# Optimization experiments

Hardware: AMD Instinct MI355X
Metric: run time of the kernel (lower is better)

## Reference

```python
import math
import jax
import jax.numpy as jnp
import numpy as np
from jax import lax

Q = 64          # num_quantiles (init default)
EPS = 1e-8      # eps (init default)


def setup_inputs() -> dict:
    key = jax.random.key(0)
    B, T, C = 64, 4096, 128
    x = jax.random.normal(key, (B, T, C), dtype=jnp.float32)
    return {"x": x}


def _build_quantile_table(x):
    """x: (B,T,C) -> quantiles (B,C,Q), levels (Q,). Unmasked branch."""
    B, T, C = x.shape
    levels = jnp.linspace(0.5 / Q, 1.0 - 0.5 / Q, Q, dtype=x.dtype)
    x_sorted = jnp.sort(x, axis=1)                      # (B,T,C) sorted over time
    positions = jnp.clip(levels * T - 0.5, 0.0, float(T - 1))   # (Q,)
    pos_int = jnp.clip(positions.astype(jnp.int32), 0, T - 2)   # (Q,)
    pos_frac = jnp.clip(positions - pos_int.astype(x.dtype), 0.0, 1.0)
    x_bct = jnp.transpose(x_sorted, (0, 2, 1))          # (B,C,T)
    q0 = x_bct[..., pos_int]                            # (B,C,Q)
    q1 = x_bct[..., jnp.minimum(pos_int + 1, T - 1)]    # (B,C,Q)
    quantiles = q0 * (1.0 - pos_frac) + q1 * pos_frac
    return quantiles, levels


def _interp_cdf(x_bc, q_bc, levels):
    """Piecewise-linear F_X(x): x_bc (N,T), q_bc (N,Q) monotone, levels (Q,)."""
    # batched searchsorted (right) per row
    idx = jax.vmap(lambda a, v: jnp.searchsorted(a, v, side="right"))(q_bc, x_bc)
    idx = jnp.clip(idx, 1, Q - 1)                       # (N,T)
    x0 = jnp.take_along_axis(q_bc, idx - 1, axis=-1)
    x1 = jnp.take_along_axis(q_bc, idx, axis=-1)
    y0 = levels[idx - 1]
    y1 = levels[idx]
    slope = (y1 - y0) / jnp.maximum(x1 - x0, 1e-12)
    return y0 + slope * (x_bc - x0)


def _probit(p):
    p_safe = jnp.clip(p, 1e-6, 1.0 - 1e-6)
    return jax.scipy.special.erfinv(2.0 * p_safe - 1.0) * math.sqrt(2.0)


def reference(x):
    B, T, C = x.shape
    quantiles, levels = _build_quantile_table(x)
    # torch detaches the quantile table: gradients flow through x only
    quantiles = lax.stop_gradient(quantiles)
    x_bc = jnp.transpose(x, (0, 2, 1)).reshape(B * C, T)
    q_bc = quantiles.reshape(B * C, Q)
    p_bc = jnp.clip(_interp_cdf(x_bc, q_bc, levels), EPS, 1.0 - EPS)
    z_bc = _probit(p_bc)
    return jnp.transpose(z_bc.reshape(B, C, T), (0, 2, 1))
```

## Files before the change

### kernel.cpp

```cpp
#include <hip/hip_runtime.h>
#include <math.h>

#define BB 64
#define TT 4096
#define CC 128
#define NQ 64
#define TCH2 128
#define NBKT 2048
#define NBKT_G 1024

__global__ __launch_bounds__(256) void transpose_kernel(const float* __restrict__ x,
                                                        float* __restrict__ xT) {
    __shared__ float tile[64][65];
    const int cb = blockIdx.x;
    const int tb = blockIdx.y;
    const int b  = blockIdx.z;
    const int tid = threadIdx.x;
    const int q = tid >> 6;
    const int l = tid & 63;

    const float* xs = x + ((size_t)b * TT + (size_t)tb * 64) * CC + (size_t)cb * 64;
    #pragma unroll
    for (int j = 0; j < 16; ++j) {
        int tl = q * 16 + j;
        tile[tl][l] = xs[(size_t)tl * CC + l];
    }
    __syncthreads();
    float* xd = xT + ((size_t)b * CC + (size_t)cb * 64) * TT + (size_t)tb * 64;
    #pragma unroll
    for (int j = 0; j < 16; ++j) {
        int cl = q * 16 + j;
        xd[(size_t)cl * TT + l] = tile[l][cl];
    }
}

__global__ __launch_bounds__(256) void bucket_quantile_T(const float* __restrict__ xT,
                                                         float* __restrict__ qtab) {
    __shared__ unsigned       A[NBKT];
    __shared__ unsigned short cum16[NBKT + 2];
    __shared__ unsigned char  flag8[NBKT];
    __shared__ unsigned short rankinfo[128];
    __shared__ unsigned short pb16[132];
    __shared__ unsigned       cur2[132];
    __shared__ unsigned       wsum[4], wsum2[4];

    const int row = blockIdx.x;
    const float* xrow = xT + (size_t)row * TT;
    const int tid = threadIdx.x, lane = tid & 63, wid = tid >> 6;

    float vv[16];
    #pragma unroll
    for (int j = 0; j < 4; ++j) {
        float4 v4 = ((const float4*)xrow)[j * 256 + tid];
        vv[j * 4 + 0] = v4.x; vv[j * 4 + 1] = v4.y;
        vv[j * 4 + 2] = v4.z; vv[j * 4 + 3] = v4.w;
    }

    *(uint4*)&A[tid * 8]      = make_uint4(0u, 0u, 0u, 0u);
    *(uint4*)&A[tid * 8 + 4]  = make_uint4(0u, 0u, 0u, 0u);
    *(uint2*)&flag8[tid * 8]  = make_uint2(~0u, ~0u);
    __syncthreads();

    #pragma unroll
    for (int j = 0; j < 16; ++j) {
        int bk = (int)((vv[j] + 5.0f) * 204.8f);
        bk = bk < 0 ? 0 : (bk > NBKT - 1 ? NBKT - 1 : bk);
        atomicAdd(&A[bk], 1u);
    }
    __syncthreads();

    uint4 h0 = *(uint4*)&A[tid * 8];
    uint4 h1 = *(uint4*)&A[tid * 8 + 4];
    unsigned S = h0.x + h0.y + h0.z + h0.w + h1.x + h1.y + h1.z + h1.w;
    unsigned incl = S;
    #pragma unroll
    for (int off = 1; off < 64; off <<= 1) {
        unsigned n = __shfl_up(incl, off, 64);
        if (lane >= off) incl += n;
    }
    if (lane == 63) wsum[wid] = incl;
    __syncthreads();
    unsigned base = incl - S;
    for (int w = 0; w < wid; ++w) base += wsum[w];

    unsigned carr[9];
    carr[0] = base;
    carr[1] = carr[0] + h0.x; carr[2] = carr[1] + h0.y;
    carr[3] = carr[2] + h0.z; carr[4] = carr[3] + h0.w;
    carr[5] = carr[4] + h1.x; carr[6] = carr[5] + h1.y;
    carr[7] = carr[6] + h1.z; carr[8] = carr[7] + h1.w;
    #pragma unroll
    for (int bi = 0; bi < 8; ++bi)
        cum16[tid * 8 + bi] = (unsigned short)carr[bi];
    if (tid == 255) cum16[NBKT] = (unsigned short)TT;

    unsigned flg = 0, myLen = 0, myCnt = 0;
    #pragma unroll
    for (int bi = 0; bi < 8; ++bi) {
        const int cs = (int)carr[bi], ce = (int)carr[bi + 1];
        if (ce > cs) {
            int t0 = cs - 32;
            int q0 = t0 < 0 ? 0 : (t0 >> 6);
            int q1 = (ce >> 6); if (q1 > 63) q1 = 63;
            bool any = false;
            for (int q = q0; q <= q1; ++q) {
                int r1 = (q << 6) + 31, r2 = r1 + 1;
                bool i1 = (r1 >= cs) && (r1 < ce);
                bool i2 = (r2 >= cs) && (r2 < ce);
                if (i1) rankinfo[2 * q]     = (unsigned short)(tid * 8 + bi);
                if (i2) rankinfo[2 * q + 1] = (unsigned short)(tid * 8 + bi);
                any |= (i1 || i2);
            }
            if (any) { flg |= (1u << bi); myLen += (unsigned)(ce - cs); myCnt++; }
        }
    }

    unsigned pk = (myLen << 16) | myCnt;
    unsigned incl2 = pk;
    #pragma unroll
    for (int off = 1; off < 64; off <<= 1) {
        unsigned n = __shfl_up(incl2, off, 64);
        if (lane >= off) incl2 += n;
    }
    if (lane == 63) wsum2[wid] = incl2;
    __syncthreads();
    unsigned b2 = incl2 - pk;
    for (int w = 0; w < wid; ++w) b2 += wsum2[w];
    unsigned lenB = b2 >> 16, cntB = b2 & 0xFFFFu;
    #pragma unroll
    for (int bi = 0; bi < 8; ++bi) {
        if (flg & (1u << bi)) {
            int s = tid * 8 + bi;
            flag8[s] = (unsigned char)cntB;
            pb16[cntB] = (unsigned short)lenB;
            cur2[cntB] = lenB;
            cntB++;
            lenB += carr[bi + 1] - carr[bi];
        }
    }
    __syncthreads();

    #pragma unroll
    for (int j = 0; j < 16; ++j) {
        int bk = (int)((vv[j] + 5.0f) * 204.8f);
        bk = bk < 0 ? 0 : (bk > NBKT - 1 ? NBKT - 1 : bk);
        unsigned char fl = flag8[bk];
        if (fl != 0xFFu) {
            unsigned p = atomicAdd(&cur2[fl], 1u);
            if (p < (unsigned)NBKT) ((float*)A)[p] = vv[j];
        }
    }
    __syncthreads();

    if (tid < 128) {
        const int j = tid;
        const int r = ((j >> 1) << 6) + 31 + (j & 1);
        const int s = rankinfo[j];
        const int cs = (int)cum16[s];
        const int L = (int)cum16[s + 1] - cs;
        const int k = r - cs;
        const unsigned char fid = flag8[s];
        const float* seg = (const float*)A + pb16[fid];

        float ans = 0.0f;
        for (int i = 0; i < L; ++i) {
            float vi = seg[i];
            int rk = 0;
            for (int jj = 0; jj < L; ++jj) {
                float vj = seg[jj];
                rk += (vj < vi) || (vj == vi && jj < i);
            }
            if (rk == k) { ans = vi; break; }
        }
        float vo = __shfl_xor(ans, 1, 64);
        if ((tid & 1) == 0)
            qtab[(size_t)row * NQ + (j >> 1)] = (ans + vo) * 0.5f;
    }
}

__global__ __launch_bounds__(256) void bucket_quantile_G(const float* __restrict__ x,
                                                         float* __restrict__ qtab) {
    __shared__ unsigned hist[NBKT_G];
    __shared__ unsigned cum[NBKT_G];
    __shared__ unsigned cur[NBKT_G];
    __shared__ float    pool[TT];
    __shared__ unsigned wsum[4];

    const int bid = blockIdx.x;
    const int row = ((bid & 7) << 10) | (bid >> 3);
    const int b = row >> 7, c = row & (CC - 1);
    const float* xrow = x + (size_t)b * TT * CC + c;
    const int tid = threadIdx.x;
    const int lane = tid & 63, wid = tid >> 6;

    float vv[16];
    #pragma unroll
    for (int j = 0; j < 16; ++j)
        vv[j] = xrow[(size_t)((j << 8) + tid) * CC];

    *(uint4*)&hist[tid << 2] = make_uint4(0u, 0u, 0u, 0u);
    __syncthreads();

    #pragma unroll
    for (int j = 0; j < 16; ++j) {
        int bk = (int)((vv[j] + 5.0f) * 102.4f);
        bk = bk < 0 ? 0 : (bk > NBKT_G - 1 ? NBKT_G - 1 : bk);
        atomicAdd(&hist[bk], 1u);
    }
    __syncthreads();

    uint4 h = *(uint4*)&hist[tid << 2];
    unsigned S = h.x + h.y + h.z + h.w;
    unsigned incl = S;
    #pragma unroll
    for (int off = 1; off < 64; off <<= 1) {
        unsigned n = __shfl_up(incl, off, 64);
        if (lane >= off) incl += n;
    }
    if (lane == 63) wsum[wid] = incl;
    __syncthreads();
    unsigned base = incl - S;
    for (int w = 0; w < wid; ++w) base += wsum[w];
    {
        unsigned c0 = base, c1 = c0 + h.x, c2 = c1 + h.y, c3 = c2 + h.z;
        *(uint4*)&cum[tid << 2] = make_uint4(c0, c1, c2, c3);
        *(uint4*)&cur[tid << 2] = make_uint4(c0, c1, c2, c3);
    }
    __syncthreads();

    #pragma unroll
    for (int j = 0; j < 16; ++j) {
        int bk = (int)((vv[j] + 5.0f) * 102.4f);
        bk = bk < 0 ? 0 : (bk > NBKT_G - 1 ? NBKT_G - 1 : bk);
        unsigned p = atomicAdd(&cur[bk], 1u);
        pool[p] = vv[j];
    }
    __syncthreads();

    if (tid < 128) {
        const int q = tid >> 1;
        const int r = (q << 6) + 31 + (tid & 1);
        int pos = 0;
        #pragma unroll
        for (int step = 512; step >= 1; step >>= 1) {
            int np = pos + step;
            if (np <= NBKT_G - 1 && (int)cum[np] <= r) pos = np;
        }
        const int segbase = (int)cum[pos];
        const int L = (int)hist[pos];
        const int k = r - segbase;
        const float* seg = &pool[segbase];

        float ans = 0.0f;
        for (int i = 0; i < L; ++i) {
            float vi = seg[i];
            int rk = 0;
            for (int jj = 0; jj < L; ++jj) {
                float vj = seg[jj];
                rk += (vj < vi) || (vj == vi && jj < i);
            }
            if (rk == k) { ans = vi; break; }
        }
        float vo = __shfl_xor(ans, 1, 64);
        if ((tid & 1) == 0)
            qtab[(size_t)row * NQ + q] = (ans + vo) * 0.5f;
    }
}

__global__ __launch_bounds__(256) void apply_kernel(const float* __restrict__ x,
                                                    const float* __restrict__ qtab,
                                                    float* __restrict__ out) {
    __shared__ float qtT[NQ][64];
    const int b   = blockIdx.x;
    const int tch = blockIdx.y;
    const int ch  = blockIdx.z;
    const int tid = threadIdx.x;

    const float* qsrc = qtab + ((size_t)b * CC + (size_t)ch * 64) * NQ;
    for (int i = tid; i < 64 * NQ; i += 256) {
        int cl = i >> 6, k = i & 63;
        qtT[k][cl ^ k] = qsrc[i];
    }
    __syncthreads();

    const int c0   = (tid & 15) * 4;
    const int trow = tid >> 4;
    const size_t base = (size_t)b * TT * CC + (size_t)tch * TCH2 * CC
                      + (size_t)ch * 64;
    const float* xp = x + base;
    float* op = out + base;
    const float invq = 1.0f / (float)NQ;

    #pragma unroll
    for (int g = 0; g < 4; ++g) {
        const int ta = trow + 16 * (2 * g);
        const int tb = trow + 16 * (2 * g + 1);
        const int offa = ta * CC + c0;
        const int offb = tb * CC + c0;
        float4 va = *(const float4*)(xp + offa);
        float4 vb = *(const float4*)(xp + offb);

        float v[8] = { va.x, va.y, va.z, va.w, vb.x, vb.y, vb.z, vb.w };
        int   cc[8];
        int   pos[8];
        #pragma unroll
        for (int e = 0; e < 8; ++e) { cc[e] = c0 + (e & 3); pos[e] = 0; }

        #pragma unroll
        for (int step = 32; step >= 1; step >>= 1) {
            float pr[8];
            #pragma unroll
            for (int e = 0; e < 8; ++e) {
                int np = pos[e] + step - 1;
                pr[e] = qtT[np][cc[e] ^ np];
            }
            #pragma unroll
            for (int e = 0; e < 8; ++e)
                if (pr[e] <= v[e]) pos[e] += step;
        }

        float x0[8], x1[8];
        #pragma unroll
        for (int e = 0; e < 8; ++e) {
            int idx = pos[e];
            idx = idx < 1 ? 1 : (idx > NQ - 1 ? NQ - 1 : idx);
            pos[e] = idx;
            x0[e] = qtT[idx - 1][cc[e] ^ (idx - 1)];
            x1[e] = qtT[idx][cc[e] ^ idx];
        }

        float r[8];
        #pragma unroll
        for (int e = 0; e < 8; ++e) {
            const float y0 = ((float)pos[e] - 0.5f) * invq;
            const float rcp = __builtin_amdgcn_rcpf(fmaxf(x1[e] - x0[e], 1e-12f));
            float p = fmaf(invq * rcp, v[e] - x0[e], y0);
            p = fminf(fmaxf(p, 1e-6f), 1.0f - 1e-6f);

            const float xx = 2.0f * p - 1.0f;
            float w = -__logf((1.0f - xx) * (1.0f + xx));
            float z;
            if (w < 5.0f) {
                float ww = w - 2.5f;
                z = 2.81022636e-08f;
                z = fmaf(z, ww, 3.43273939e-07f);
                z = fmaf(z, ww, -3.5233877e-06f);
                z = fmaf(z, ww, -4.39150654e-06f);
                z = fmaf(z, ww, 0.00021858087f);
                z = fmaf(z, ww, -0.00125372503f);
                z = fmaf(z, ww, -0.00417768164f);
                z = fmaf(z, ww, 0.246640727f);
                z = fmaf(z, ww, 1.50140941f);
            } else {
                float ww = sqrtf(w) - 3.0f;
                z = -0.000200214257f;
                z = fmaf(z, ww, 0.000100950558f);
                z = fmaf(z, ww, 0.00134934322f);
                z = fmaf(z, ww, -0.00367342844f);
                z = fmaf(z, ww, 0.00573950773f);
                z = fmaf(z, ww, -0.0076224613f);
                z = fmaf(z, ww, 0.00943887047f);
                z = fmaf(z, ww, 1.00167406f);
                z = fmaf(z, ww, 2.83297682f);
            }
            r[e] = z * xx * 1.4142135623730951f;
        }

        *(float4*)(op + offa) = make_float4(r[0], r[1], r[2], r[3]);
        *(float4*)(op + offb) = make_float4(r[4], r[5], r[6], r[7]);
    }
}

extern "C" void kernel_launch(void* const* d_in, const int* in_sizes, int n_in,
                              void* d_out, int out_size, void* d_ws, size_t ws_size,
                              hipStream_t stream) {
    const float* x = (const float*)d_in[0];
    float* out = (float*)d_out;
    float* qtab = (float*)d_ws;
    const size_t qtab_bytes = (size_t)BB * CC * NQ * 4;
    const size_t xT_bytes   = (size_t)BB * CC * TT * 4;

    if (ws_size >= qtab_bytes + xT_bytes) {
        float* xT = (float*)((char*)d_ws + qtab_bytes);
        dim3 tgrid(2, 64, BB);
        transpose_kernel<<<tgrid, 256, 0, stream>>>(x, xT);
        bucket_quantile_T<<<BB * CC, 256, 0, stream>>>(xT, qtab);
    } else {
        bucket_quantile_G<<<BB * CC, 256, 0, stream>>>(x, qtab);
    }
    dim3 grid(BB, TT / TCH2, 2);
    apply_kernel<<<grid, 256, 0, stream>>>(x, qtab, out);
}
```

Baseline: 216.7 us.

## Shrink quantile blocks to 128 threads, reload row instead of holding registers

The bucket-quantile kernel now runs with 128 threads per row, each handling 16 histogram bins and 32 values. The values are read from global memory a second time in the scatter pass instead of being kept in registers. The cumulative-count table is removed by packing each bin's index and in-bin rank into rankinfo, with bin lengths stored in a new len8 array. The aim is lower shared memory and register use per block for better occupancy and fewer barriers, at the cost of a second global read of each row and less parallelism within a block.

```diff
diff --git a/kernel.cpp b/kernel.cpp
--- a/kernel.cpp
+++ b/kernel.cpp
@@ -34,44 +34,48 @@
     }
 }
 
-__global__ __launch_bounds__(256) void bucket_quantile_T(const float* __restrict__ xT,
+__global__ __launch_bounds__(128) void bucket_quantile_T(const float* __restrict__ xT,
                                                          float* __restrict__ qtab) {
     __shared__ unsigned       A[NBKT];
-    __shared__ unsigned short cum16[NBKT + 2];
     __shared__ unsigned char  flag8[NBKT];
-    __shared__ unsigned short rankinfo[128];
+    __shared__ unsigned       rankinfo[128];
     __shared__ unsigned short pb16[132];
+    __shared__ unsigned char  len8[132];
     __shared__ unsigned       cur2[132];
-    __shared__ unsigned       wsum[4], wsum2[4];
+    __shared__ unsigned       wsum[2], wsum2[2];
 
     const int row = blockIdx.x;
     const float* xrow = xT + (size_t)row * TT;
     const int tid = threadIdx.x, lane = tid & 63, wid = tid >> 6;
 
-    float vv[16];
-    #pragma unroll
-    for (int j = 0; j < 4; ++j) {
-        float4 v4 = ((const float4*)xrow)[j * 256 + tid];
-        vv[j * 4 + 0] = v4.x; vv[j * 4 + 1] = v4.y;
-        vv[j * 4 + 2] = v4.z; vv[j * 4 + 3] = v4.w;
-    }
-
-    *(uint4*)&A[tid * 8]      = make_uint4(0u, 0u, 0u, 0u);
-    *(uint4*)&A[tid * 8 + 4]  = make_uint4(0u, 0u, 0u, 0u);
-    *(uint2*)&flag8[tid * 8]  = make_uint2(~0u, ~0u);
-    __syncthreads();
-
-    #pragma unroll
-    for (int j = 0; j < 16; ++j) {
-        int bk = (int)((vv[j] + 5.0f) * 204.8f);
-        bk = bk < 0 ? 0 : (bk > NBKT - 1 ? NBKT - 1 : bk);
-        atomicAdd(&A[bk], 1u);
-    }
-    __syncthreads();
-
-    uint4 h0 = *(uint4*)&A[tid * 8];
-    uint4 h1 = *(uint4*)&A[tid * 8 + 4];
-    unsigned S = h0.x + h0.y + h0.z + h0.w + h1.x + h1.y + h1.z + h1.w;
+    #pragma unroll
+    for (int q = 0; q < 4; ++q)
+        *(uint4*)&A[tid * 16 + q * 4] = make_uint4(0u, 0u, 0u, 0u);
+    *(uint4*)&flag8[tid * 16] = make_uint4(~0u, ~0u, ~0u, ~0u);
+    __syncthreads();
+
+    #pragma unroll
+    for (int j = 0; j < 8; ++j) {
+        float4 v4 = ((const float4*)xrow)[j * 128 + tid];
+        int b0 = (int)((v4.x + 5.0f) * 204.8f); b0 = b0 < 0 ? 0 : (b0 > NBKT-1 ? NBKT-1 : b0);
+        int b1 = (int)((v4.y + 5.0f) * 204.8f); b1 = b1 < 0 ? 0 : (b1 > NBKT-1 ? NBKT-1 : b1);
+        int b2 = (int)((v4.z + 5.0f) * 204.8f); b2 = b2 < 0 ? 0 : (b2 > NBKT-1 ? NBKT-1 : b2);
+        int b3 = (int)((v4.w + 5.0f) * 204.8f); b3 = b3 < 0 ? 0 : (b3 > NBKT-1 ? NBKT-1 : b3);
+        atomicAdd(&A[b0], 1u); atomicAdd(&A[b1], 1u);
+        atomicAdd(&A[b2], 1u); atomicAdd(&A[b3], 1u);
+    }
+    __syncthreads();
+
+    unsigned hh[16];
+    #pragma unroll
+    for (int q = 0; q < 4; ++q) {
+        uint4 t4 = *(uint4*)&A[tid * 16 + q * 4];
+        hh[q * 4 + 0] = t4.x; hh[q * 4 + 1] = t4.y;
+        hh[q * 4 + 2] = t4.z; hh[q * 4 + 3] = t4.w;
+    }
+    unsigned S = 0;
+    #pragma unroll
+    for (int i = 0; i < 16; ++i) S += hh[i];
     unsigned incl = S;
     #pragma unroll
     for (int off = 1; off < 64; off <<= 1) {
@@ -80,23 +84,16 @@
     }
     if (lane == 63) wsum[wid] = incl;
     __syncthreads();
-    unsigned base = incl - S;
-    for (int w = 0; w < wid; ++w) base += wsum[w];
-
-    unsigned carr[9];
+    unsigned base = incl - S + ((wid == 1) ? wsum[0] : 0u);
+
+    unsigned carr[17];
     carr[0] = base;
-    carr[1] = carr[0] + h0.x; carr[2] = carr[1] + h0.y;
-    carr[3] = carr[2] + h0.z; carr[4] = carr[3] + h0.w;
-    carr[5] = carr[4] + h1.x; carr[6] = carr[5] + h1.y;
-    carr[7] = carr[6] + h1.z; carr[8] = carr[7] + h1.w;
-    #pragma unroll
-    for (int bi = 0; bi < 8; ++bi)
-        cum16[tid * 8 + bi] = (unsigned short)carr[bi];
-    if (tid == 255) cum16[NBKT] = (unsigned short)TT;
+    #pragma unroll
+    for (int i = 0; i < 16; ++i) carr[i + 1] = carr[i] + hh[i];
 
     unsigned flg = 0, myLen = 0, myCnt = 0;
     #pragma unroll
-    for (int bi = 0; bi < 8; ++bi) {
+    for (int bi = 0; bi < 16; ++bi) {
         const int cs = (int)carr[bi], ce = (int)carr[bi + 1];
         if (ce > cs) {
             int t0 = cs - 32;
@@ -107,8 +104,9 @@
                 int r1 = (q << 6) + 31, r2 = r1 + 1;
                 bool i1 = (r1 >= cs) && (r1 < ce);
                 bool i2 = (r2 >= cs) && (r2 < ce);
-                if (i1) rankinfo[2 * q]     = (unsigned short)(tid * 8 + bi);
-                if (i2) rankinfo[2 * q + 1] = (unsigned short)(tid * 8 + bi);
+                unsigned sbin = (unsigned)(tid * 16 + bi);
+                if (i1) rankinfo[2 * q]     = (sbin << 8) | (unsigned)(r1 - cs);
+                if (i2) rankinfo[2 * q + 1] = (sbin << 8) | (unsigned)(r2 - cs);
                 any |= (i1 || i2);
             }
             if (any) { flg |= (1u << bi); myLen += (unsigned)(ce - cs); myCnt++; }
@@ -124,42 +122,47 @@
     }
     if (lane == 63) wsum2[wid] = incl2;
     __syncthreads();
-    unsigned b2 = incl2 - pk;
-    for (int w = 0; w < wid; ++w) b2 += wsum2[w];
+    unsigned b2 = incl2 - pk + ((wid == 1) ? wsum2[0] : 0u);
     unsigned lenB = b2 >> 16, cntB = b2 & 0xFFFFu;
     #pragma unroll
-    for (int bi = 0; bi < 8; ++bi) {
+    for (int bi = 0; bi < 16; ++bi) {
         if (flg & (1u << bi)) {
-            int s = tid * 8 + bi;
+            int s = tid * 16 + bi;
+            unsigned L = carr[bi + 1] - carr[bi];
             flag8[s] = (unsigned char)cntB;
             pb16[cntB] = (unsigned short)lenB;
+            len8[cntB] = (unsigned char)(L > 255u ? 255u : L);
             cur2[cntB] = lenB;
             cntB++;
-            lenB += carr[bi + 1] - carr[bi];
-        }
-    }
-    __syncthreads();
-
-    #pragma unroll
-    for (int j = 0; j < 16; ++j) {
-        int bk = (int)((vv[j] + 5.0f) * 204.8f);
-        bk = bk < 0 ? 0 : (bk > NBKT - 1 ? NBKT - 1 : bk);
-        unsigned char fl = flag8[bk];
-        if (fl != 0xFFu) {
-            unsigned p = atomicAdd(&cur2[fl], 1u);
-            if (p < (unsigned)NBKT) ((float*)A)[p] = vv[j];
-        }
-    }
-    __syncthreads();
-
-    if (tid < 128) {
+            lenB += L;
+        }
+    }
+    __syncthreads();
+
+    #pragma unroll
+    for (int j = 0; j < 8; ++j) {
+        float4 v4 = ((const float4*)xrow)[j * 128 + tid];
+        float vs[4] = { v4.x, v4.y, v4.z, v4.w };
+        #pragma unroll
+        for (int e = 0; e < 4; ++e) {
+            int bk = (int)((vs[e] + 5.0f) * 204.8f);
+            bk = bk < 0 ? 0 : (bk > NBKT - 1 ? NBKT - 1 : bk);
+            unsigned char fl = flag8[bk];
+            if (fl != 0xFFu) {
+                unsigned p = atomicAdd(&cur2[fl], 1u);
+                if (p < (unsigned)NBKT) ((float*)A)[p] = vs[e];
+            }
+        }
+    }
+    __syncthreads();
+
+    {
         const int j = tid;
-        const int r = ((j >> 1) << 6) + 31 + (j & 1);
-        const int s = rankinfo[j];
-        const int cs = (int)cum16[s];
-        const int L = (int)cum16[s + 1] - cs;
-        const int k = r - cs;
+        const unsigned info = rankinfo[j];
+        const int s = (int)(info >> 8);
+        const int k = (int)(info & 0xFFu);
         const unsigned char fid = flag8[s];
+        const int L = (int)len8[fid];
         const float* seg = (const float*)A + pb16[fid];
 
         float ans = 0.0f;
@@ -384,7 +387,7 @@
         float* xT = (float*)((char*)d_ws + qtab_bytes);
         dim3 tgrid(2, 64, BB);
         transpose_kernel<<<tgrid, 256, 0, stream>>>(x, xT);
-        bucket_quantile_T<<<BB * CC, 256, 0, stream>>>(xT, qtab);
+        bucket_quantile_T<<<BB * CC, 128, 0, stream>>>(xT, qtab);
     } else {
         bucket_quantile_G<<<BB * CC, 256, 0, stream>>>(x, qtab);
     }
```

New measurement: 226.4 us. 4.5% more time.
